# Performance work log

Hardware: AMD Instinct MI355X
Metric: run time of the kernel (lower is better)

Reference implementation:

```python
import jax, jax.numpy as jnp
import numpy as np

E, W, C, N, Q = 8, 5, 640, 49, 75


def setup_inputs() -> dict:
    key = jax.random.key(0)
    k1, k2 = jax.random.split(key)
    proto = jax.random.normal(k1, (E, W, C, 1, N), dtype=jnp.float32)
    query = jax.random.normal(k2, (E, Q, C, 1, N), dtype=jnp.float32)
    return {"proto": proto, "query": query}


def reference(proto, query):
    # proto: [E, W, C, 1, N] -> [E, W, C, N]; query: [E, Q, C, 1, N] -> [E, Q, C, N]
    p = jnp.squeeze(proto, axis=3)
    q = jnp.squeeze(query, axis=3)
    # cosine similarity map over channel dim C:
    # sim[e,q,w,n,m] = <p[e,w,:,n], q[e,q,:,m]>
    sim = jnp.einsum('ewcn,eqcm->eqwnm', p, q)
    norm_p = jnp.linalg.norm(p, axis=2)  # [E, W, N]
    norm_q = jnp.linalg.norm(q, axis=2)  # [E, Q, N]
    denom = norm_p[:, None, :, :, None] * norm_q[:, :, None, None, :] + 1e-8
    return sim / denom  # [E, Q, W, N, N]
```

## Files before the change

kernel.cpp:

```cpp
#include <hip/hip_runtime.h>
#include <hip/hip_bf16.h>


#define E_CNT 8
#define W_CNT 5
#define C_CNT 640
#define N_CNT 49
#define Q_CNT 75
#define QM_TOT (Q_CNT * N_CNT)
#define MROWS (W_CNT * N_CNT)
#define NTILES 29
#define ASW_BLK 32768
#define ASW_SIZE (E_CNT * 10 * ASW_BLK)
#define PN_OFF ASW_SIZE
#define PN_PART_BYTES (E_CNT * 10 * MROWS * 4)
#define WS_NEEDED ((size_t)(PN_OFF + PN_PART_BYTES))

#define AB_OFF 0
#define B_OFF 65536
#define QN_OFF 98304
#define PNL_OFF 98816
#define SM_BYTES 99840

typedef __attribute__((ext_vector_type(8))) short bf16x8;
typedef __attribute__((ext_vector_type(4))) float f32x4;

static __device__ __forceinline__ short f2bf(float f) {
    __hip_bfloat16 h = __float2bfloat16(f);
    return *reinterpret_cast<short*>(&h);
}

static __device__ __forceinline__ void gload16(const void* g, void* l) {
    __builtin_amdgcn_global_load_lds(
        (const __attribute__((address_space(1))) void*)g,
        (__attribute__((address_space(3))) void*)l, 16, 0, 0);
}

__global__ __launch_bounds__(256, 4)
void prep_kernel(const float* __restrict__ proto,
                 unsigned char* __restrict__ asw,
                 float* __restrict__ pn_part)
{
    __shared__ float pns[MROWS];
    const int b = blockIdx.x;
    const int e = b / 10, cc = b % 10;
    const float* pbase = proto + (size_t)e * (W_CNT * C_CNT * N_CNT);
    unsigned char* abase = asw + (size_t)(e * 10 + cc) * ASW_BLK;
    const int t = threadIdx.x;
    if (t < MROWS) pns[t] = 0.f;
    __syncthreads();

    #pragma unroll
    for (int i = 0; i < 8; ++i) {
        const int s = t + i * 256;
        if (s < 8 * MROWS) {
            const int kb = s / MROWS;
            const int nw = s - kb * MROWS;
            const int w = nw / N_CNT, n = nw - w * N_CNT;
            const float* g = pbase + ((size_t)(w * C_CNT + cc * 64 + kb * 8)) * N_CNT + n;
            float vv[8];
            #pragma unroll
            for (int j = 0; j < 8; ++j) vv[j] = g[(size_t)j * N_CNT];
            float ss = 0.f;
            bf16x8 pk;
            #pragma unroll
            for (int j = 0; j < 8; ++j) { const float f = vv[j]; ss += f * f; pk[j] = f2bf(f); }
            *reinterpret_cast<bf16x8*>(abase + nw * 128 + ((kb ^ (nw & 7)) << 4)) = pk;
            atomicAdd(&pns[nw], ss);
        } else {
            const int x = s - 8 * MROWS;
            const int nw = MROWS + (x >> 3), kb = x & 7;
            *reinterpret_cast<bf16x8*>(abase + nw * 128 + ((kb ^ (nw & 7)) << 4)) =
                (bf16x8){0, 0, 0, 0, 0, 0, 0, 0};
        }
    }
    __syncthreads();
    if (t < MROWS) pn_part[(size_t)(e * 10 + cc) * MROWS + t] = pns[t];
}

__global__ __launch_bounds__(512, 2)
void gemm_kernel(const float* __restrict__ query,
                 const unsigned char* __restrict__ asw,
                 const float* __restrict__ pn_part,
                 float* __restrict__ out)
{
    extern __shared__ unsigned char sm[];
    const int b = blockIdx.x;
    const int e = b / NTILES, jt = b - e * NTILES;
    const int qm0 = jt * 128;
    const int t = threadIdx.x;
    const int wv = t >> 6, ln = t & 63;
    const int lrow = ln & 15, lk = ln >> 4;
    const int wm = wv >> 1, wn = wv & 1;

    float* qn = (float*)(sm + QN_OFF);
    float* pnl = (float*)(sm + PNL_OFF);
    if (t < 128) qn[t] = 0.f;

    const int r = t & 127;
    const int kb0 = t >> 7;
    const int qm = qm0 + r;
    const bool valid = qm < QM_TOT;
    const int q = valid ? (qm / N_CNT) : 0;
    const int m = qm - q * N_CNT;
    const float* qsrc = query + ((size_t)(e * Q_CNT + q) * C_CNT) * N_CNT + m;
    const int bo0 = r * 128 + (((kb0)     ^ (r & 7)) << 4);
    const int bo1 = r * 128 + (((kb0 + 4) ^ (r & 7)) << 4);

    const unsigned char* agl = asw + (size_t)(e * 10) * ASW_BLK;

    float vb[2][8];
    float ss_tot = 0.f;

    f32x4 acc[4][4];
    #pragma unroll
    for (int i = 0; i < 4; ++i)
        #pragma unroll
        for (int j = 0; j < 4; ++j) acc[i][j] = (f32x4){0.f, 0.f, 0.f, 0.f};

#define A_ISSUE(cc, buf) do {                                                   \
    const unsigned char* ag_ = agl + (size_t)(cc) * ASW_BLK;                    \
    _Pragma("unroll")                                                           \
    for (int i_ = 0; i_ < 4; ++i_)                                              \
        gload16(ag_ + (t + i_ * 512) * 16, sm + (buf) * 32768 + (t + i_ * 512) * 16); \
} while (0)

#define B_ISSUE(cc) do {                                                        \
    _Pragma("unroll")                                                           \
    for (int i_ = 0; i_ < 2; ++i_) {                                            \
        const size_t co_ = (size_t)((cc) * 64 + (kb0 + i_ * 4) * 8) * N_CNT;    \
        _Pragma("unroll")                                                       \
        for (int j_ = 0; j_ < 8; ++j_)                                          \
            vb[i_][j_] = valid ? qsrc[co_ + (size_t)j_ * N_CNT] : 0.f;          \
    }                                                                           \
} while (0)

#define B_WRITE(buf) do {                                                       \
    _Pragma("unroll")                                                           \
    for (int i_ = 0; i_ < 2; ++i_) {                                            \
        bf16x8 pk_; float s8_ = 0.f;                                            \
        _Pragma("unroll")                                                       \
        for (int j_ = 0; j_ < 8; ++j_) {                                        \
            const float f_ = vb[i_][j_]; s8_ += f_ * f_; pk_[j_] = f2bf(f_);    \
        }                                                                       \
        ss_tot += s8_;                                                          \
        *reinterpret_cast<bf16x8*>(sm + B_OFF + (buf) * 16384 + (i_ ? bo1 : bo0)) = pk_; \
    }                                                                           \
} while (0)

    A_ISSUE(0, 0);
    B_ISSUE(0);
    B_WRITE(0);
    __syncthreads();

    for (int cc = 0; cc < 10; ++cc) {
        const int cur = cc & 1, nxt = cur ^ 1;
        if (cc < 9) { A_ISSUE(cc + 1, nxt); B_ISSUE(cc + 1); }

        {
            const unsigned char* Ab = sm + cur * 32768;
            const unsigned char* Bb = sm + B_OFF + cur * 16384;
            #pragma unroll
            for (int ks = 0; ks < 2; ++ks) {
                bf16x8 af[4], bfr[4];
                #pragma unroll
                for (int i = 0; i < 4; ++i) {
                    const int row = wm * 64 + i * 16 + lrow;
                    const int gr = (ks * 4 + lk) ^ (row & 7);
                    af[i] = *reinterpret_cast<const bf16x8*>(Ab + row * 128 + gr * 16);
                }
                #pragma unroll
                for (int j = 0; j < 4; ++j) {
                    const int cl = wn * 64 + j * 16 + lrow;
                    const int gr = (ks * 4 + lk) ^ (cl & 7);
                    bfr[j] = *reinterpret_cast<const bf16x8*>(Bb + cl * 128 + gr * 16);
                }
                #pragma unroll
                for (int i = 0; i < 4; ++i)
                    #pragma unroll
                    for (int j = 0; j < 4; ++j)
                        acc[i][j] = __builtin_amdgcn_mfma_f32_16x16x32_bf16(
                            af[i], bfr[j], acc[i][j], 0, 0, 0);
            }
        }

        if (cc < 9) B_WRITE(nxt);
        __syncthreads();
    }

    atomicAdd(&qn[r], ss_tot);
    if (t < MROWS) {
        float s = 0.f;
        #pragma unroll
        for (int cc = 0; cc < 10; ++cc) s += pn_part[(size_t)(e * 10 + cc) * MROWS + t];
        pnl[t] = sqrtf(s);
    }
    __syncthreads();

    float nq4[4];
    int cl4[4];
    #pragma unroll
    for (int j = 0; j < 4; ++j) {
        cl4[j] = wn * 64 + j * 16 + lrow;
        nq4[j] = sqrtf(qn[cl4[j]]);
    }
    #pragma unroll
    for (int i = 0; i < 4; ++i) {
        #pragma unroll
        for (int rr = 0; rr < 4; ++rr) {
            const int nw = wm * 64 + i * 16 + lk * 4 + rr;
            if (nw < MROWS) {
                const float np_ = pnl[nw];
                const int w = nw / N_CNT, n = nw - w * N_CNT;
                #pragma unroll
                for (int j = 0; j < 4; ++j) {
                    const int qmj = qm0 + cl4[j];
                    if (qmj < QM_TOT) {
                        const int qq = qmj / N_CNT, mm = qmj - qq * N_CNT;
                        const float den = np_ * nq4[j] + 1e-8f;
                        out[(((size_t)(e * Q_CNT + qq) * W_CNT + w) * N_CNT + n) * N_CNT + mm] =
                            acc[i][j][rr] * __builtin_amdgcn_rcpf(den);
                    }
                }
            }
        }
    }
#undef A_ISSUE
#undef B_ISSUE
#undef B_WRITE
}

struct SMemFB {
    unsigned char A[256 * 128];
    unsigned char B[64 * 128];
    float ns[320];
};

__global__ __launch_bounds__(512, 4)
void sim_fallback_kernel(const float* __restrict__ proto,
                         const float* __restrict__ query,
                         float* __restrict__ out)
{
    __shared__ SMemFB smf;
    const int t = threadIdx.x;
    const int e = blockIdx.x / Q_CNT;
    const int q = blockIdx.x - e * Q_CNT;
    const float* pbase = proto + (size_t)e * (W_CNT * C_CNT * N_CNT);
    const float* qbase = query + ((size_t)e * Q_CNT + q) * (C_CNT * N_CNT);
    unsigned char* lds = (unsigned char*)&smf;
    if (t < 320) smf.ns[t] = 0.f;
    if (t < 208) {
        if (t < 88) *reinterpret_cast<f32x4*>(smf.A + 245 * 128 + t * 16) = (f32x4){0.f,0.f,0.f,0.f};
        else        *reinterpret_cast<f32x4*>(smf.B + 49 * 128 + (t - 88) * 16) = (f32x4){0.f,0.f,0.f,0.f};
    }
    const int nslot5 = (t < 304);
    const float* gp[5];
    int offidx[5];
    #pragma unroll
    for (int i = 0; i < 5; ++i) {
        gp[i] = pbase; offidx[i] = 0;
        if (i < 4 || nslot5) {
            const int s = t + i * 512;
            if (s < 1960) {
                const int kb = s / 245, nw = s - kb * 245;
                const int w = nw / 49, n = nw - w * 49;
                gp[i] = pbase + ((size_t)w * C_CNT + kb * 8) * N_CNT + n;
                offidx[i] = (nw * 128 + ((kb ^ (nw & 7)) << 4)) | (nw << 16);
            } else {
                const int s2 = s - 1960;
                const int kb = s2 / 49, mq = s2 - kb * 49;
                gp[i] = qbase + (size_t)(kb * 8) * N_CNT + mq;
                offidx[i] = (32768 + mq * 128 + ((kb ^ (mq & 7)) << 4)) | ((256 + mq) << 16);
            }
        }
    }
    float v[5][8];
    float ss[5] = {0.f,0.f,0.f,0.f,0.f};
    #pragma unroll
    for (int i = 0; i < 4; ++i)
        #pragma unroll
        for (int j = 0; j < 8; ++j) v[i][j] = gp[i][(size_t)j * N_CNT];
    if (nslot5)
        #pragma unroll
        for (int j = 0; j < 8; ++j) v[4][j] = gp[4][(size_t)j * N_CNT];
    f32x4 acc[2][4];
    #pragma unroll
    for (int i = 0; i < 2; ++i)
        #pragma unroll
        for (int j = 0; j < 4; ++j) acc[i][j] = (f32x4){0.f,0.f,0.f,0.f};
    const int wv = t >> 6, ln = t & 63, lrow = ln & 15, lk = ln >> 4;
    for (int kc = 0; kc < 10; ++kc) {
        #pragma unroll
        for (int i = 0; i < 5; ++i) {
            if (i < 4 || nslot5) {
                bf16x8 pk; float s8 = 0.f;
                #pragma unroll
                for (int j = 0; j < 8; ++j) { const float f = v[i][j]; s8 += f*f; pk[j] = f2bf(f); }
                ss[i] += s8;
                *reinterpret_cast<bf16x8*>(lds + (offidx[i] & 0xFFFF)) = pk;
            }
        }
        __syncthreads();
        if (kc < 9) {
            #pragma unroll
            for (int i = 0; i < 4; ++i) {
                gp[i] += 64 * N_CNT;
                #pragma unroll
                for (int j = 0; j < 8; ++j) v[i][j] = gp[i][(size_t)j * N_CNT];
            }
            if (nslot5) {
                gp[4] += 64 * N_CNT;
                #pragma unroll
                for (int j = 0; j < 8; ++j) v[4][j] = gp[4][(size_t)j * N_CNT];
            }
        }
        #pragma unroll
        for (int ks = 0; ks < 2; ++ks) {
            bf16x8 af[2], bfr[4];
            #pragma unroll
            for (int i = 0; i < 2; ++i) {
                const int row = (wv * 2 + i) * 16 + lrow;
                const int gr = (ks * 4 + lk) ^ (row & 7);
                af[i] = *reinterpret_cast<const bf16x8*>(lds + row * 128 + gr * 16);
            }
            #pragma unroll
            for (int j = 0; j < 4; ++j) {
                const int mq = j * 16 + lrow;
                const int gr = (ks * 4 + lk) ^ (mq & 7);
                bfr[j] = *reinterpret_cast<const bf16x8*>(lds + 32768 + mq * 128 + gr * 16);
            }
            #pragma unroll
            for (int i = 0; i < 2; ++i)
                #pragma unroll
                for (int j = 0; j < 4; ++j)
                    acc[i][j] = __builtin_amdgcn_mfma_f32_16x16x32_bf16(af[i], bfr[j], acc[i][j], 0, 0, 0);
        }
        __syncthreads();
    }
    #pragma unroll
    for (int i = 0; i < 5; ++i)
        if (i < 4 || nslot5) atomicAdd(&smf.ns[offidx[i] >> 16], ss[i]);
    __syncthreads();
    float nq[4];
    #pragma unroll
    for (int j = 0; j < 4; ++j) {
        const int mq = j * 16 + lrow;
        nq[j] = (mq < N_CNT) ? sqrtf(smf.ns[256 + mq]) : 1.f;
    }
    float* obase = out + (size_t)(e * Q_CNT + q) * (W_CNT * N_CNT * N_CNT);
    #pragma unroll
    for (int i = 0; i < 2; ++i) {
        #pragma unroll
        for (int rr = 0; rr < 4; ++rr) {
            const int nw = (wv * 2 + i) * 16 + lk * 4 + rr;
            if (nw < W_CNT * N_CNT) {
                const int w = nw / 49, n = nw - w * 49;
                const float np_ = sqrtf(smf.ns[nw]);
                float* orow = obase + ((size_t)w * N_CNT + n) * N_CNT;
                #pragma unroll
                for (int j = 0; j < 4; ++j) {
                    const int mq = j * 16 + lrow;
                    if (mq < N_CNT) orow[mq] = acc[i][j][rr] / (np_ * nq[j] + 1e-8f);
                }
            }
        }
    }
}

extern "C" void kernel_launch(void* const* d_in, const int* in_sizes, int n_in,
                              void* d_out, int out_size, void* d_ws, size_t ws_size,
                              hipStream_t stream)
{
    const float* proto = (const float*)d_in[0];
    const float* query = (const float*)d_in[1];
    float* out = (float*)d_out;

    if (ws_size < WS_NEEDED) {
        hipLaunchKernelGGL(sim_fallback_kernel, dim3(E_CNT * Q_CNT), dim3(512), 0, stream,
                           proto, query, out);
        return;
    }

    unsigned char* asw = (unsigned char*)d_ws;
    float* pn_part = (float*)((unsigned char*)d_ws + PN_OFF);

    hipLaunchKernelGGL(prep_kernel, dim3(E_CNT * 10), dim3(256), 0, stream,
                       proto, asw, pn_part);
    hipLaunchKernelGGL(gemm_kernel, dim3(E_CNT * NTILES), dim3(512), SM_BYTES, stream,
                       query, asw, pn_part, out);
}
```

Measured before the change: 40.78 us.

## Halve GEMM column tile to 64 and prefetch query loads two chunks ahead

The gemm kernel now uses 64-column query tiles with 256 threads, four waves each covering 64 proto rows, and a grid of 464 blocks instead of 232. The intent is to fill more of the GPU's compute units with this small problem. Global loads of the query are now issued two K-chunks ahead into a double register buffer, giving them more time to arrive, and the norm scratch reuses the A region after the loop. The cost is that each proto A tile is loaded twice as often across blocks, and register pressure rises from the larger prefetch buffer.

After: 64.53 us. +58.2%, slower.

```diff
diff --git a/kernel.cpp b/kernel.cpp
--- a/kernel.cpp
+++ b/kernel.cpp
@@ -9,18 +9,15 @@
 #define Q_CNT 75
 #define QM_TOT (Q_CNT * N_CNT)
 #define MROWS (W_CNT * N_CNT)
-#define NTILES 29
+#define NT64 58
 #define ASW_BLK 32768
 #define ASW_SIZE (E_CNT * 10 * ASW_BLK)
 #define PN_OFF ASW_SIZE
 #define PN_PART_BYTES (E_CNT * 10 * MROWS * 4)
 #define WS_NEEDED ((size_t)(PN_OFF + PN_PART_BYTES))
 
-#define AB_OFF 0
 #define B_OFF 65536
-#define QN_OFF 98304
-#define PNL_OFF 98816
-#define SM_BYTES 99840
+#define SM_BYTES 81920
 
 typedef __attribute__((ext_vector_type(8))) short bf16x8;
 typedef __attribute__((ext_vector_type(4))) float f32x4;
@@ -78,7 +75,7 @@
     if (t < MROWS) pn_part[(size_t)(e * 10 + cc) * MROWS + t] = pns[t];
 }
 
-__global__ __launch_bounds__(512, 2)
+__global__ __launch_bounds__(256, 2)
 void gemm_kernel(const float* __restrict__ query,
                  const unsigned char* __restrict__ asw,
                  const float* __restrict__ pn_part,
@@ -86,30 +83,26 @@
 {
     extern __shared__ unsigned char sm[];
     const int b = blockIdx.x;
-    const int e = b / NTILES, jt = b - e * NTILES;
-    const int qm0 = jt * 128;
+    const int e = b & 7;
+    const int jt = b >> 3;
+    const int qm0 = jt * 64;
     const int t = threadIdx.x;
     const int wv = t >> 6, ln = t & 63;
     const int lrow = ln & 15, lk = ln >> 4;
-    const int wm = wv >> 1, wn = wv & 1;
-
-    float* qn = (float*)(sm + QN_OFF);
-    float* pnl = (float*)(sm + PNL_OFF);
-    if (t < 128) qn[t] = 0.f;
-
-    const int r = t & 127;
-    const int kb0 = t >> 7;
+
+    const int r = t & 63;
+    const int kb0 = t >> 6;
     const int qm = qm0 + r;
     const bool valid = qm < QM_TOT;
     const int q = valid ? (qm / N_CNT) : 0;
-    const int m = qm - q * N_CNT;
-    const float* qsrc = query + ((size_t)(e * Q_CNT + q) * C_CNT) * N_CNT + m;
-    const int bo0 = r * 128 + (((kb0)     ^ (r & 7)) << 4);
+    const int m = valid ? (qm - q * N_CNT) : 0;
+    const float* qsrc = query + (size_t)(e * Q_CNT + q) * (C_CNT * N_CNT) + m;
+    const int bo0 = r * 128 + ((kb0 ^ (r & 7)) << 4);
     const int bo1 = r * 128 + (((kb0 + 4) ^ (r & 7)) << 4);
 
     const unsigned char* agl = asw + (size_t)(e * 10) * ASW_BLK;
 
-    float vb[2][8];
+    float vb[2][16];
     float ss_tot = 0.f;
 
     f32x4 acc[4][4];
@@ -121,57 +114,59 @@
 #define A_ISSUE(cc, buf) do {                                                   \
     const unsigned char* ag_ = agl + (size_t)(cc) * ASW_BLK;                    \
     _Pragma("unroll")                                                           \
-    for (int i_ = 0; i_ < 4; ++i_)                                              \
-        gload16(ag_ + (t + i_ * 512) * 16, sm + (buf) * 32768 + (t + i_ * 512) * 16); \
+    for (int i_ = 0; i_ < 8; ++i_)                                              \
+        gload16(ag_ + (t + i_ * 256) * 16, sm + (buf) * 32768 + (t + i_ * 256) * 16); \
 } while (0)
 
-#define B_ISSUE(cc) do {                                                        \
+#define B_LOAD(cc, slot) do {                                                   \
     _Pragma("unroll")                                                           \
-    for (int i_ = 0; i_ < 2; ++i_) {                                            \
-        const size_t co_ = (size_t)((cc) * 64 + (kb0 + i_ * 4) * 8) * N_CNT;    \
+    for (int h_ = 0; h_ < 2; ++h_) {                                            \
+        const size_t co_ = (size_t)((cc) * 64 + (kb0 + h_ * 4) * 8) * N_CNT;    \
         _Pragma("unroll")                                                       \
         for (int j_ = 0; j_ < 8; ++j_)                                          \
-            vb[i_][j_] = valid ? qsrc[co_ + (size_t)j_ * N_CNT] : 0.f;          \
+            vb[slot][h_ * 8 + j_] = valid ? qsrc[co_ + (size_t)j_ * N_CNT] : 0.f; \
     }                                                                           \
 } while (0)
 
-#define B_WRITE(buf) do {                                                       \
+#define B_WRITE(slot, buf) do {                                                 \
     _Pragma("unroll")                                                           \
-    for (int i_ = 0; i_ < 2; ++i_) {                                            \
+    for (int h_ = 0; h_ < 2; ++h_) {                                            \
         bf16x8 pk_; float s8_ = 0.f;                                            \
         _Pragma("unroll")                                                       \
         for (int j_ = 0; j_ < 8; ++j_) {                                        \
-            const float f_ = vb[i_][j_]; s8_ += f_ * f_; pk_[j_] = f2bf(f_);    \
+            const float f_ = vb[slot][h_ * 8 + j_]; s8_ += f_ * f_; pk_[j_] = f2bf(f_); \
         }                                                                       \
         ss_tot += s8_;                                                          \
-        *reinterpret_cast<bf16x8*>(sm + B_OFF + (buf) * 16384 + (i_ ? bo1 : bo0)) = pk_; \
+        *reinterpret_cast<bf16x8*>(sm + B_OFF + (buf) * 8192 + (h_ ? bo1 : bo0)) = pk_; \
     }                                                                           \
 } while (0)
 
+    B_LOAD(0, 0);
+    B_LOAD(1, 1);
     A_ISSUE(0, 0);
-    B_ISSUE(0);
-    B_WRITE(0);
+    B_WRITE(0, 0);
     __syncthreads();
 
     for (int cc = 0; cc < 10; ++cc) {
         const int cur = cc & 1, nxt = cur ^ 1;
-        if (cc < 9) { A_ISSUE(cc + 1, nxt); B_ISSUE(cc + 1); }
+        if (cc < 9) A_ISSUE(cc + 1, nxt);
+        if (cc < 8) B_LOAD(cc + 2, cur);
 
         {
             const unsigned char* Ab = sm + cur * 32768;
-            const unsigned char* Bb = sm + B_OFF + cur * 16384;
+            const unsigned char* Bb = sm + B_OFF + cur * 8192;
             #pragma unroll
             for (int ks = 0; ks < 2; ++ks) {
                 bf16x8 af[4], bfr[4];
                 #pragma unroll
                 for (int i = 0; i < 4; ++i) {
-                    const int row = wm * 64 + i * 16 + lrow;
+                    const int row = wv * 64 + i * 16 + lrow;
                     const int gr = (ks * 4 + lk) ^ (row & 7);
                     af[i] = *reinterpret_cast<const bf16x8*>(Ab + row * 128 + gr * 16);
                 }
                 #pragma unroll
                 for (int j = 0; j < 4; ++j) {
-                    const int cl = wn * 64 + j * 16 + lrow;
+                    const int cl = j * 16 + lrow;
                     const int gr = (ks * 4 + lk) ^ (cl & 7);
                     bfr[j] = *reinterpret_cast<const bf16x8*>(Bb + cl * 128 + gr * 16);
                 }
@@ -184,10 +179,14 @@
             }
         }
 
-        if (cc < 9) B_WRITE(nxt);
+        if (cc < 9) B_WRITE(nxt, nxt);
         __syncthreads();
     }
 
+    float* qn = (float*)sm;
+    float* pnl = (float*)(sm + 256);
+    if (t < 64) qn[t] = 0.f;
+    __syncthreads();
     atomicAdd(&qn[r], ss_tot);
     if (t < MROWS) {
         float s = 0.f;
@@ -201,14 +200,14 @@
     int cl4[4];
     #pragma unroll
     for (int j = 0; j < 4; ++j) {
-        cl4[j] = wn * 64 + j * 16 + lrow;
+        cl4[j] = j * 16 + lrow;
         nq4[j] = sqrtf(qn[cl4[j]]);
     }
     #pragma unroll
     for (int i = 0; i < 4; ++i) {
         #pragma unroll
         for (int rr = 0; rr < 4; ++rr) {
-            const int nw = wm * 64 + i * 16 + lk * 4 + rr;
+            const int nw = wv * 64 + i * 16 + lk * 4 + rr;
             if (nw < MROWS) {
                 const float np_ = pnl[nw];
                 const int w = nw / N_CNT, n = nw - w * N_CNT;
@@ -226,7 +225,7 @@
         }
     }
 #undef A_ISSUE
-#undef B_ISSUE
+#undef B_LOAD
 #undef B_WRITE
 }
 
@@ -386,6 +385,6 @@
 
     hipLaunchKernelGGL(prep_kernel, dim3(E_CNT * 10), dim3(256), 0, stream,
                        proto, asw, pn_part);
-    hipLaunchKernelGGL(gemm_kernel, dim3(E_CNT * NTILES), dim3(512), SM_BYTES, stream,
+    hipLaunchKernelGGL(gemm_kernel, dim3(E_CNT * NT64), dim3(256), SM_BYTES, stream,
                        query, asw, pn_part, out);
 }
```
